# Kernel optimization log

Measured on AMD Instinct MI355X. Metric: run time of the kernel, lower is better.

The kernel has to match this reference:

```python
import jax, jax.numpy as jnp
import numpy as np

IH, IW = 32, 32
HEADS = 8
DIM_HEAD = 32
INNER = HEADS * DIM_HEAD  # 256
INP = 256
OUP = 256
SCALE = DIM_HEAD ** -0.5


def _relative_index(ih, iw):
    # Reproduce the torch buffer computation (meshgrid indexing='ij').
    yy, xx = np.meshgrid(np.arange(ih), np.arange(iw), indexing='ij')
    coords = np.stack([yy.ravel(), xx.ravel()])            # [2, n]
    rel = coords[:, :, None] - coords[:, None, :]          # [2, n, n]
    rel[0] += ih - 1
    rel[1] += iw - 1
    rel[0] *= 2 * iw - 1
    idx = rel.sum(0).ravel()                               # [n*n]
    return jnp.asarray(idx, dtype=jnp.int32)


def setup_inputs() -> dict:
    key = jax.random.key(0)
    k1, k2, k3, k4 = jax.random.split(key, 4)
    B, N = 16, IH * IW
    x = jax.random.normal(k1, (B, N, INP), dtype=jnp.float32)
    # Parameters (stored as [in, out] so forward is x @ W).
    W_qkv = jax.random.normal(k2, (INP, 3 * INNER), dtype=jnp.float32) * 0.02
    W_out = jax.random.normal(k3, (INNER, OUP), dtype=jnp.float32) * 0.02
    b_out = jnp.zeros((OUP,), dtype=jnp.float32)
    bias_table = jax.random.normal(k4, ((2 * IH - 1) * (2 * IW - 1), HEADS), dtype=jnp.float32) * 0.02
    rel_index = _relative_index(IH, IW)
    return {"x": x, "W_qkv": W_qkv, "W_out": W_out, "b_out": b_out,
            "bias_table": bias_table, "rel_index": rel_index}


def reference(x, W_qkv, W_out, b_out, bias_table, rel_index):
    B, N, _ = x.shape
    qkv = x @ W_qkv                                        # [B, N, 3*inner]
    q, k, v = jnp.split(qkv, 3, axis=-1)
    def to_heads(t):  # b n (h d) -> b h n d
        return t.reshape(B, N, HEADS, DIM_HEAD).transpose(0, 2, 1, 3)
    q, k, v = to_heads(q), to_heads(k), to_heads(v)
    dots = jnp.einsum('bhnd,bhmd->bhnm', q, k) * SCALE     # [B, H, N, N]
    # Gather relative position bias: [n*n, heads] -> [1, heads, n, n]
    rel_bias = bias_table[rel_index].reshape(N, N, HEADS).transpose(2, 0, 1)
    dots = dots + rel_bias[None]
    attn = jax.nn.softmax(dots, axis=-1)
    out = jnp.einsum('bhnm,bhmd->bhnd', attn, v)           # [B, H, N, D]
    out = out.transpose(0, 2, 1, 3).reshape(B, N, INNER)   # b n (h d)
    return out @ W_out + b_out
```

## Files before the change

kernel.cpp:

```cpp
#include <hip/hip_runtime.h>
#include <stdint.h>
#include <stddef.h>


typedef _Float16 f16;
typedef __attribute__((ext_vector_type(8))) _Float16 half8;
typedef __attribute__((ext_vector_type(4))) _Float16 half4;
typedef __attribute__((ext_vector_type(2))) __fp16 fp16x2;
typedef __attribute__((ext_vector_type(4))) float f32x4;

#define MFMA16(a, b, c) __builtin_amdgcn_mfma_f32_16x16x32_f16((a), (b), (c), 0, 0, 0)

__global__ __launch_bounds__(256) void prep_kernel(
    const float* __restrict__ x,
    const float* __restrict__ W_qkv, const float* __restrict__ W_out,
    const float* __restrict__ bias_table, const int* __restrict__ rel_index,
    f16* __restrict__ Wtq, f16* __restrict__ Wto, f16* __restrict__ ebC,
    f16* __restrict__ xh)
{
  (void)rel_index;
  const float kLog2e = 1.4426950408889634f;
  const float kScale = 0.17677669529663687f * kLog2e;
  int tid = blockIdx.x * 256 + threadIdx.x;
  if (tid < 24576) {
    int c = tid >> 5;
    int k8 = (tid & 31) << 3;
    float s = (c < 256) ? kScale : 1.0f;
    f16* dst = Wtq + c * 256 + k8;
#pragma unroll
    for (int j = 0; j < 8; ++j)
      dst[j] = (f16)(W_qkv[(k8 + j) * 768 + c] * s);
  } else if (tid < 32768) {
    int t = tid - 24576;
    int c = t >> 5;
    int k8 = (t & 31) << 3;
    f16* dst = Wto + c * 256 + k8;
#pragma unroll
    for (int j = 0; j < 8; ++j)
      dst[j] = (f16)W_out[(k8 + j) * 256 + c];
  } else if (tid < 97280) {
    int t = tid - 32768;
    int e = t * 8;
    int h = e / 64512;
    int r = e - h * 64512;
    int dy = r >> 10;
    int xi = (r >> 5) & 31;
    int xj0 = r & 31;
    int base = dy * 63 + xi + 31;
    f16* dst = ebC + e;
#pragma unroll
    for (int j = 0; j < 8; ++j)
      dst[j] = (f16)__expf(bias_table[(base - (xj0 + j)) * 8 + h]);
  } else {
    int t = tid - 97280;
    const float* src = x + (size_t)t * 8;
    f16* dst = xh + (size_t)t * 8;
#pragma unroll
    for (int j = 0; j < 8; ++j) dst[j] = (f16)src[j];
  }
}

__global__ __launch_bounds__(256, 4) void qkv_kernel(
    const f16* __restrict__ xh, const f16* __restrict__ Wt,
    f16* __restrict__ Qh, f16* __restrict__ Kh, f16* __restrict__ Vt)
{
  __shared__ f16 Bs[64 * 256];
  int mt = blockIdx.x, nt = blockIdx.y;
  int tid = threadIdx.x;
  int wave = tid >> 6, lane = tid & 63;
  int g = lane >> 4, q16 = lane & 15;
  int cbase = nt * 64;
  char* BsB = (char*)Bs;
  const f16* WtG = Wt + (size_t)cbase * 256;
#pragma unroll
  for (int i = 0; i < 8; ++i) {
    int c = i * 256 + tid;
    int row = c >> 5;
    int colb = (c & 31) << 4;
    half8 v = *(const half8*)(WtG + c * 8);
    *(half8*)(BsB + row * 512 + (colb ^ ((row & 7) << 4))) = v;
  }
  __syncthreads();

  int rbase = mt * 128 + wave * 32;
  const f16* xr0 = xh + (size_t)(rbase + q16) * 256 + g * 8;
  f32x4 acc[2][4] = {};
#pragma unroll 2
  for (int kc = 0; kc < 8; ++kc) {
    half8 bf[4];
#pragma unroll
    for (int cf = 0; cf < 4; ++cf) {
      int row = cf * 16 + q16;
      int colb = kc * 64 + g * 16;
      bf[cf] = *(const half8*)(BsB + row * 512 + (colb ^ ((row & 7) << 4)));
    }
#pragma unroll
    for (int mf = 0; mf < 2; ++mf) {
      half8 af = *(const half8*)(xr0 + (size_t)(mf * 16) * 256 + kc * 32);
#pragma unroll
      for (int cf = 0; cf < 4; ++cf)
        acc[mf][cf] = MFMA16(af, bf[cf], acc[mf][cf]);
    }
  }

#pragma unroll
  for (int mf = 0; mf < 2; ++mf) {
#pragma unroll
    for (int cf = 0; cf < 4; ++cf) {
      int c = cbase + cf * 16 + q16;
      int which = c >> 8, h = (c >> 5) & 7, d = c & 31;
      int m0 = rbase + mf * 16 + g * 4;
      int b = m0 >> 10, n0 = m0 & 1023;
      size_t bh = (size_t)(b * 8 + h);
      if (which == 2) {
        half4 vv;
#pragma unroll
        for (int r = 0; r < 4; ++r) vv[r] = (f16)acc[mf][cf][r];
        *(half4*)(Vt + (((bh << 5) | d) << 10) + n0) = vv;
      } else {
        f16* base = (which == 0) ? Qh : Kh;
#pragma unroll
        for (int r = 0; r < 4; ++r)
          base[((bh << 10) | (n0 + r)) * 32 + d] = (f16)acc[mf][cf][r];
      }
    }
  }
}

__global__ __launch_bounds__(256) void attn_kernel(
    const f16* __restrict__ Qh, const f16* __restrict__ Kh,
    const f16* __restrict__ Vt, const f16* __restrict__ ebC,
    f16* __restrict__ Oh)
{
  int bid = blockIdx.x;
  int h = bid & 7;
  int rest = bid >> 3;
  int qt = rest & 3;
  int b = rest >> 2;
  int wave = threadIdx.x >> 6, lane = threadIdx.x & 63;
  int g = lane >> 4, q16 = lane & 15;
  int bh = b * 8 + h;
  int qbase = qt * 256 + wave * 64;
  const f16* Qb = Qh + ((size_t)bh << 15);
  const f16* Kb = Kh + ((size_t)bh << 15);
  const f16* Vb = Vt + ((size_t)bh << 15);

  half8 qf0 = *(const half8*)(Qb + (size_t)(qbase +  0 + q16) * 32 + g * 8);
  half8 qf1 = *(const half8*)(Qb + (size_t)(qbase + 16 + q16) * 32 + g * 8);
  half8 qf2 = *(const half8*)(Qb + (size_t)(qbase + 32 + q16) * 32 + g * 8);
  half8 qf3 = *(const half8*)(Qb + (size_t)(qbase + 48 + q16) * 32 + g * 8);

  int kr0 = ((q16 >> 2) << 3) | (q16 & 3);
  const f16* Kp0 = Kb + kr0 * 32 + g * 8;
  const f16* Kp1 = Kp0 + 4 * 32;
  const f16* Vp0 = Vb + (size_t)q16 * 1024 + g * 8;
  const f16* Vp1 = Vb + (size_t)(16 + q16) * 1024 + g * 8;
  int yi0 = qbase >> 5;
  const f16* Bp = ebC + ((((h * 63 + yi0 + 31) * 32 + q16) << 5) + g * 8);

  f32x4 o0a = {0.f,0.f,0.f,0.f}, o1a = {0.f,0.f,0.f,0.f};
  f32x4 o0b = {0.f,0.f,0.f,0.f}, o1b = {0.f,0.f,0.f,0.f};
  f32x4 o0c = {0.f,0.f,0.f,0.f}, o1c = {0.f,0.f,0.f,0.f};
  f32x4 o0d = {0.f,0.f,0.f,0.f}, o1d = {0.f,0.f,0.f,0.f};
  float lsa = 0.f, lsb = 0.f, lsc = 0.f, lsd = 0.f;
  const fp16x2 one2 = {(__fp16)1.0f, (__fp16)1.0f};
  (void)one2;

#if __has_builtin(__builtin_amdgcn_fdot2)
#define LSUM(LS, PU)                                                         \
    LS = __builtin_amdgcn_fdot2(PU.h2[0], one2, LS, false);                  \
    LS = __builtin_amdgcn_fdot2(PU.h2[1], one2, LS, false);                  \
    LS = __builtin_amdgcn_fdot2(PU.h2[2], one2, LS, false);                  \
    LS = __builtin_amdgcn_fdot2(PU.h2[3], one2, LS, false);
#else
#define LSUM(LS, PU)                                                         \
    _Pragma("unroll") for (int i = 0; i < 8; ++i) { LS += (float)PU.h8[i]; }
#endif

#define FRAG_BODY(QF, K0, K1, V0, V1, EB, O0, O1, LS)                        \
  {                                                                          \
    const f32x4 zz = {0.f, 0.f, 0.f, 0.f};                                   \
    f32x4 s0 = MFMA16(K0, QF, zz);              \
    f32x4 s1 = MFMA16(K1, QF, zz);                         \
    union { fp16x2 h2[4]; half8 h8; } pu, eu;                                \
    eu.h8 = EB;                                                              \
    pu.h2[0] = __builtin_amdgcn_cvt_pkrtz(                                   \
        __builtin_amdgcn_exp2f(s0[0]), __builtin_amdgcn_exp2f(s0[1]));       \
    pu.h2[1] = __builtin_amdgcn_cvt_pkrtz(                                   \
        __builtin_amdgcn_exp2f(s0[2]), __builtin_amdgcn_exp2f(s0[3]));       \
    pu.h2[2] = __builtin_amdgcn_cvt_pkrtz(                                   \
        __builtin_amdgcn_exp2f(s1[0]), __builtin_amdgcn_exp2f(s1[1]));       \
    pu.h2[3] = __builtin_amdgcn_cvt_pkrtz(                                   \
        __builtin_amdgcn_exp2f(s1[2]), __builtin_amdgcn_exp2f(s1[3]));       \
    pu.h2[0] *= eu.h2[0];  pu.h2[1] *= eu.h2[1];           \
    pu.h2[2] *= eu.h2[2];  pu.h2[3] *= eu.h2[3];                             \
    LSUM(LS, pu)                                                             \
    O0 = MFMA16(V0, pu.h8, O0);                          \
    O1 = MFMA16(V1, pu.h8, O1);                       \
  }

  half8 kA0 = *(const half8*)Kp0;
  half8 kA1 = *(const half8*)Kp1;
  half8 vA0 = *(const half8*)Vp0;
  half8 vA1 = *(const half8*)Vp1;
  half8 bA0 = *(const half8*)(Bp);
  half8 bA1 = *(const half8*)(Bp + 512);
  half8 bA2 = *(const half8*)(Bp + 1024);
  half8 bA3 = *(const half8*)(Bp + 1536);

  for (int kt = 0; kt < 31; ++kt) {
    size_t ko = (size_t)(kt + 1) * 1024;
    int    co = (kt + 1) * 32;
    const f16* Bn = Bp - ko;
    half8 kB0 = *(const half8*)(Kp0 + ko);
    half8 kB1 = *(const half8*)(Kp1 + ko);
    half8 vB0 = *(const half8*)(Vp0 + co);
    half8 vB1 = *(const half8*)(Vp1 + co);
    half8 bB0 = *(const half8*)(Bn);
    half8 bB1 = *(const half8*)(Bn + 512);
    half8 bB2 = *(const half8*)(Bn + 1024);
    half8 bB3 = *(const half8*)(Bn + 1536);
    __builtin_amdgcn_sched_barrier(0);
    FRAG_BODY(qf0, kA0, kA1, vA0, vA1, bA0, o0a, o1a, lsa);
    FRAG_BODY(qf1, kA0, kA1, vA0, vA1, bA1, o0b, o1b, lsb);
    FRAG_BODY(qf2, kA0, kA1, vA0, vA1, bA2, o0c, o1c, lsc);
    FRAG_BODY(qf3, kA0, kA1, vA0, vA1, bA3, o0d, o1d, lsd);
    kA0 = kB0; kA1 = kB1; vA0 = vB0; vA1 = vB1;
    bA0 = bB0; bA1 = bB1; bA2 = bB2; bA3 = bB3;
  }
  FRAG_BODY(qf0, kA0, kA1, vA0, vA1, bA0, o0a, o1a, lsa);
  FRAG_BODY(qf1, kA0, kA1, vA0, vA1, bA1, o0b, o1b, lsb);
  FRAG_BODY(qf2, kA0, kA1, vA0, vA1, bA2, o0c, o1c, lsc);
  FRAG_BODY(qf3, kA0, kA1, vA0, vA1, bA3, o0d, o1d, lsd);
#undef FRAG_BODY
#undef LSUM

#define FRAG_OUT(O0, O1, LS, FOFF)                                           \
  {                                                                          \
    float l = LS;                                                            \
    l += __shfl_xor(l, 16);                                                  \
    l += __shfl_xor(l, 32);                                                  \
    float invl = 1.0f / l;                                                   \
    f16* op = Oh + (((size_t)bh << 10) + qbase + (FOFF) + q16) * 32;         \
    half4 w0, w1;                                                            \
    _Pragma("unroll") for (int r = 0; r < 4; ++r) {                          \
      w0[r] = (f16)(O0[r] * invl); w1[r] = (f16)(O1[r] * invl);              \
    }                                                                        \
    *(half4*)(op + g * 4) = w0;                                              \
    *(half4*)(op + 16 + g * 4) = w1;                                         \
  }
  FRAG_OUT(o0a, o1a, lsa, 0);
  FRAG_OUT(o0b, o1b, lsb, 16);
  FRAG_OUT(o0c, o1c, lsc, 32);
  FRAG_OUT(o0d, o1d, lsd, 48);
#undef FRAG_OUT
}

__global__ __launch_bounds__(256, 4) void out_kernel(
    const f16* __restrict__ Oh, const f16* __restrict__ Wto,
    const float* __restrict__ b_out, float* __restrict__ out)
{
  __shared__ f16 Bs[32 * 256];
  int mt = blockIdx.x, nt = blockIdx.y;
  int tid = threadIdx.x;
  int wave = tid >> 6, lane = tid & 63;
  int g = lane >> 4, q16 = lane & 15;
  int cbase = nt * 32;
  char* BsB = (char*)Bs;
  const f16* WtG = Wto + (size_t)cbase * 256;
#pragma unroll
  for (int i = 0; i < 4; ++i) {
    int c = i * 256 + tid;
    int row = c >> 5;
    int colb = (c & 31) << 4;
    half8 v = *(const half8*)(WtG + c * 8);
    *(half8*)(BsB + row * 512 + (colb ^ ((row & 7) << 4))) = v;
  }
  __syncthreads();

  int rbase = mt * 128 + wave * 32;
  int b = rbase >> 10;
  int nb = rbase & 1023;
  f32x4 acc[2][2] = {};
#pragma unroll 2
  for (int kc = 0; kc < 8; ++kc) {
    half8 bf[2];
#pragma unroll
    for (int cf = 0; cf < 2; ++cf) {
      int row = cf * 16 + q16;
      int colb = kc * 64 + g * 16;
      bf[cf] = *(const half8*)(BsB + row * 512 + (colb ^ ((row & 7) << 4)));
    }
#pragma unroll
    for (int mf = 0; mf < 2; ++mf) {
      int n = nb + mf * 16 + q16;
      half8 af = *(const half8*)(Oh + ((((size_t)(b * 8 + kc)) << 10) | n) * 32 + g * 8);
#pragma unroll
      for (int cf = 0; cf < 2; ++cf)
        acc[mf][cf] = MFMA16(af, bf[cf], acc[mf][cf]);
    }
  }

#pragma unroll
  for (int mf = 0; mf < 2; ++mf) {
#pragma unroll
    for (int cf = 0; cf < 2; ++cf) {
      int c = cbase + cf * 16 + q16;
      float bias = b_out[c];
#pragma unroll
      for (int r = 0; r < 4; ++r) {
        int mm = rbase + mf * 16 + g * 4 + r;
        out[(size_t)mm * 256 + c] = acc[mf][cf][r] + bias;
      }
    }
  }
}

extern "C" void kernel_launch(void* const* d_in, const int* in_sizes, int n_in,
                              void* d_out, int out_size, void* d_ws, size_t ws_size,
                              hipStream_t stream) {
  (void)in_sizes; (void)n_in; (void)out_size; (void)ws_size;
  const float* x        = (const float*)d_in[0];
  const float* W_qkv    = (const float*)d_in[1];
  const float* W_out    = (const float*)d_in[2];
  const float* b_out    = (const float*)d_in[3];
  const float* bias_tab = (const float*)d_in[4];
  const int*   rel_idx  = (const int*)d_in[5];
  float* out = (float*)d_out;
  char* ws = (char*)d_ws;

  f16* Qh  = (f16*)(ws);
  f16* Kh  = (f16*)(ws + (size_t)(8u  << 20));
  f16* Vt  = (f16*)(ws + (size_t)(16u << 20));
  f16* ebC = (f16*)(ws + (size_t)(24u << 20));
  f16* xh  = (f16*)(ws + (size_t)(40u << 20));
  f16* Oh  = (f16*)(ws + (size_t)(40u << 20));
  f16* Wtq = (f16*)(ws + (size_t)(48u << 20));
  f16* Wto = (f16*)(ws + (size_t)(48u << 20) + 768 * 256 * 2);

  hipLaunchKernelGGL(prep_kernel, dim3(2428), dim3(256), 0, stream,
                     x, W_qkv, W_out, bias_tab, rel_idx, Wtq, Wto, ebC, xh);
  hipLaunchKernelGGL(qkv_kernel, dim3(128, 12), dim3(256), 0, stream,
                     xh, Wtq, Qh, Kh, Vt);
  hipLaunchKernelGGL(attn_kernel, dim3(512), dim3(256), 0, stream,
                     Qh, Kh, Vt, ebC, Oh);
  hipLaunchKernelGGL(out_kernel, dim3(128, 8), dim3(256), 0, stream,
                     Oh, Wto, b_out, out);
}
```

Measured before the change: 81.87 us.

## Fuse attention with output projection via shared-memory head outputs

After: 78.09 us. 4.6% less time.

```diff
diff --git a/kernel.cpp b/kernel.cpp
--- a/kernel.cpp
+++ b/kernel.cpp
@@ -14,11 +14,10 @@
 __global__ __launch_bounds__(256) void prep_kernel(
     const float* __restrict__ x,
     const float* __restrict__ W_qkv, const float* __restrict__ W_out,
-    const float* __restrict__ bias_table, const int* __restrict__ rel_index,
+    const float* __restrict__ bias_table,
     f16* __restrict__ Wtq, f16* __restrict__ Wto, f16* __restrict__ ebC,
     f16* __restrict__ xh)
 {
-  (void)rel_index;
   const float kLog2e = 1.4426950408889634f;
   const float kScale = 0.17677669529663687f * kLog2e;
   int tid = blockIdx.x * 256 + threadIdx.x;
@@ -127,20 +126,21 @@
   }
 }
 
-__global__ __launch_bounds__(256) void attn_kernel(
+__global__ __launch_bounds__(512) void attn_out_kernel(
     const f16* __restrict__ Qh, const f16* __restrict__ Kh,
     const f16* __restrict__ Vt, const f16* __restrict__ ebC,
-    f16* __restrict__ Oh)
+    const f16* __restrict__ Wto, const float* __restrict__ b_out,
+    float* __restrict__ out)
 {
+  __shared__ f16 Os[8 * 64 * 32];
   int bid = blockIdx.x;
-  int h = bid & 7;
-  int rest = bid >> 3;
-  int qt = rest & 3;
-  int b = rest >> 2;
+  int b = bid & 15;
+  int qt = bid >> 4;
   int wave = threadIdx.x >> 6, lane = threadIdx.x & 63;
   int g = lane >> 4, q16 = lane & 15;
+  int h = wave;
   int bh = b * 8 + h;
-  int qbase = qt * 256 + wave * 64;
+  int qbase = qt * 64;
   const f16* Qb = Qh + ((size_t)bh << 15);
   const f16* Kb = Kh + ((size_t)bh << 15);
   const f16* Vb = Vt + ((size_t)bh << 15);
@@ -235,81 +235,58 @@
 #undef FRAG_BODY
 #undef LSUM
 
-#define FRAG_OUT(O0, O1, LS, FOFF)                                           \
+  char* OsB = (char*)Os + h * 4096;
+#define FRAG_OUT(O0, O1, LS, F)                                              \
   {                                                                          \
     float l = LS;                                                            \
     l += __shfl_xor(l, 16);                                                  \
     l += __shfl_xor(l, 32);                                                  \
     float invl = 1.0f / l;                                                   \
-    f16* op = Oh + (((size_t)bh << 10) + qbase + (FOFF) + q16) * 32;         \
+    int floc = (F) * 16 + q16;                                               \
+    int swz = (floc & 7) << 4;                                               \
     half4 w0, w1;                                                            \
     _Pragma("unroll") for (int r = 0; r < 4; ++r) {                          \
       w0[r] = (f16)(O0[r] * invl); w1[r] = (f16)(O1[r] * invl);              \
     }                                                                        \
-    *(half4*)(op + g * 4) = w0;                                              \
-    *(half4*)(op + 16 + g * 4) = w1;                                         \
+    *(half4*)(OsB + ((floc * 64 + g * 8) ^ swz)) = w0;                       \
+    *(half4*)(OsB + ((floc * 64 + 32 + g * 8) ^ swz)) = w1;                  \
   }
   FRAG_OUT(o0a, o1a, lsa, 0);
-  FRAG_OUT(o0b, o1b, lsb, 16);
-  FRAG_OUT(o0c, o1c, lsc, 32);
-  FRAG_OUT(o0d, o1d, lsd, 48);
+  FRAG_OUT(o0b, o1b, lsb, 1);
+  FRAG_OUT(o0c, o1c, lsc, 2);
+  FRAG_OUT(o0d, o1d, lsd, 3);
 #undef FRAG_OUT
-}
-
-__global__ __launch_bounds__(256, 4) void out_kernel(
-    const f16* __restrict__ Oh, const f16* __restrict__ Wto,
-    const float* __restrict__ b_out, float* __restrict__ out)
-{
-  __shared__ f16 Bs[32 * 256];
-  int mt = blockIdx.x, nt = blockIdx.y;
-  int tid = threadIdx.x;
-  int wave = tid >> 6, lane = tid & 63;
-  int g = lane >> 4, q16 = lane & 15;
-  int cbase = nt * 32;
-  char* BsB = (char*)Bs;
-  const f16* WtG = Wto + (size_t)cbase * 256;
-#pragma unroll
-  for (int i = 0; i < 4; ++i) {
-    int c = i * 256 + tid;
-    int row = c >> 5;
-    int colb = (c & 31) << 4;
-    half8 v = *(const half8*)(WtG + c * 8);
-    *(half8*)(BsB + row * 512 + (colb ^ ((row & 7) << 4))) = v;
-  }
+
   __syncthreads();
 
-  int rbase = mt * 128 + wave * 32;
-  int b = rbase >> 10;
-  int nb = rbase & 1023;
-  f32x4 acc[2][2] = {};
-#pragma unroll 2
+  int cb = wave * 32;
+  float bias0 = b_out[cb + q16];
+  float bias1 = b_out[cb + 16 + q16];
+  f32x4 acc[4][2] = {};
+  const char* OsA = (const char*)Os;
+#pragma unroll
   for (int kc = 0; kc < 8; ++kc) {
-    half8 bf[2];
+    half8 bf0 = *(const half8*)(Wto + (size_t)(cb + q16) * 256 + kc * 32 + g * 8);
+    half8 bf1 = *(const half8*)(Wto + (size_t)(cb + 16 + q16) * 256 + kc * 32 + g * 8);
+#pragma unroll
+    for (int mf = 0; mf < 4; ++mf) {
+      int row = mf * 16 + q16;
+      half8 af = *(const half8*)(OsA + kc * 4096 +
+                                 ((row * 64 + g * 16) ^ ((row & 7) << 4)));
+      acc[mf][0] = MFMA16(af, bf0, acc[mf][0]);
+      acc[mf][1] = MFMA16(af, bf1, acc[mf][1]);
+    }
+  }
+
+#pragma unroll
+  for (int mf = 0; mf < 4; ++mf) {
 #pragma unroll
     for (int cf = 0; cf < 2; ++cf) {
-      int row = cf * 16 + q16;
-      int colb = kc * 64 + g * 16;
-      bf[cf] = *(const half8*)(BsB + row * 512 + (colb ^ ((row & 7) << 4)));
-    }
-#pragma unroll
-    for (int mf = 0; mf < 2; ++mf) {
-      int n = nb + mf * 16 + q16;
-      half8 af = *(const half8*)(Oh + ((((size_t)(b * 8 + kc)) << 10) | n) * 32 + g * 8);
-#pragma unroll
-      for (int cf = 0; cf < 2; ++cf)
-        acc[mf][cf] = MFMA16(af, bf[cf], acc[mf][cf]);
-    }
-  }
-
-#pragma unroll
-  for (int mf = 0; mf < 2; ++mf) {
-#pragma unroll
-    for (int cf = 0; cf < 2; ++cf) {
-      int c = cbase + cf * 16 + q16;
-      float bias = b_out[c];
+      int c = cb + cf * 16 + q16;
+      float bias = cf ? bias1 : bias0;
 #pragma unroll
       for (int r = 0; r < 4; ++r) {
-        int mm = rbase + mf * 16 + g * 4 + r;
+        int mm = (b << 10) + qbase + mf * 16 + g * 4 + r;
         out[(size_t)mm * 256 + c] = acc[mf][cf][r] + bias;
       }
     }
@@ -325,7 +302,6 @@
   const float* W_out    = (const float*)d_in[2];
   const float* b_out    = (const float*)d_in[3];
   const float* bias_tab = (const float*)d_in[4];
-  const int*   rel_idx  = (const int*)d_in[5];
   float* out = (float*)d_out;
   char* ws = (char*)d_ws;
 
@@ -334,16 +310,13 @@
   f16* Vt  = (f16*)(ws + (size_t)(16u << 20));
   f16* ebC = (f16*)(ws + (size_t)(24u << 20));
   f16* xh  = (f16*)(ws + (size_t)(40u << 20));
-  f16* Oh  = (f16*)(ws + (size_t)(40u << 20));
   f16* Wtq = (f16*)(ws + (size_t)(48u << 20));
   f16* Wto = (f16*)(ws + (size_t)(48u << 20) + 768 * 256 * 2);
 
   hipLaunchKernelGGL(prep_kernel, dim3(2428), dim3(256), 0, stream,
-                     x, W_qkv, W_out, bias_tab, rel_idx, Wtq, Wto, ebC, xh);
+                     x, W_qkv, W_out, bias_tab, Wtq, Wto, ebC, xh);
   hipLaunchKernelGGL(qkv_kernel, dim3(128, 12), dim3(256), 0, stream,
                      xh, Wtq, Qh, Kh, Vt);
-  hipLaunchKernelGGL(attn_kernel, dim3(512), dim3(256), 0, stream,
-                     Qh, Kh, Vt, ebC, Oh);
-  hipLaunchKernelGGL(out_kernel, dim3(128, 8), dim3(256), 0, stream,
-                     Oh, Wto, b_out, out);
+  hipLaunchKernelGGL(attn_out_kernel, dim3(256), dim3(512), 0, stream,
+                     Qh, Kh, Vt, ebC, Wto, b_out, out);
 }
```
